# Kernel optimization log

Hardware: AMD Instinct MI355X
Metric: run time of the kernel (lower is better)

The kernel has to match this reference:

```python
import jax, jax.numpy as jnp
import numpy as np

B, Q, A, D = 32, 48, 48, 300   # batch, question len, answer len, word embed dim
C, K = 512, 5                  # conv out channels, kernel height
H, P, NCLS = 512, 512, 2       # hidden_size, projection_size, n_classes
EPS_COS = 1e-6
EPS_BN = 1e-5


def _simple_cnn(x, conv_w, conv_b, fc_w, fc_b):
    # x: (N, L, D) -> Conv2d(1->C, kernel=(K, D), padding=(K-1, 0)) -> relu -> maxpool over length -> fc
    y = jax.lax.conv_general_dilated(
        x[:, None, :, :], conv_w, window_strides=(1, 1),
        padding=((K - 1, K - 1), (0, 0)),
        dimension_numbers=('NCHW', 'OIHW', 'NCHW'))  # (N, C, L+K-1, 1)
    y = jax.nn.relu(y + conv_b[None, :, None, None])[..., 0]  # (N, C, L')
    y = jnp.max(y, axis=2)                                    # (N, C)  max_pool1d over full length
    return y @ fc_w.T + fc_b                                  # (N, H)


def setup_inputs() -> dict:
    key = jax.random.key(0)
    ks = jax.random.split(key, 12)
    s = lambda n: 1.0 / np.sqrt(n)
    return {
        'a_features': jax.random.normal(ks[0], (B, Q, D), jnp.float32),
        'b_features': jax.random.normal(ks[1], (B, A, D), jnp.float32),
        'sm_conv_w': jax.random.normal(ks[2], (C, 1, K, D), jnp.float32) * s(K * D),
        'sm_conv_b': jnp.zeros((C,), jnp.float32),
        'sm_fc_w': jax.random.normal(ks[3], (H, C), jnp.float32) * s(C),
        'sm_fc_b': jnp.zeros((H,), jnp.float32),
        'ctx_conv_w': jax.random.normal(ks[4], (C, 1, K, D), jnp.float32) * s(K * D),
        'ctx_conv_b': jnp.zeros((C,), jnp.float32),
        'ctx_fc_w': jax.random.normal(ks[5], (H, C), jnp.float32) * s(C),
        'ctx_fc_b': jnp.zeros((H,), jnp.float32),
        'proj_w': jax.random.normal(ks[6], (P, 3 * H), jnp.float32) * s(3 * H),
        'proj_b': jnp.zeros((P,), jnp.float32),
        'bn_gamma': jnp.ones((P,), jnp.float32),
        'bn_beta': jnp.zeros((P,), jnp.float32),
        'out_w': jax.random.normal(ks[7], (NCLS, P), jnp.float32) * s(P),
        'out_b': jnp.zeros((NCLS,), jnp.float32),
    }


def reference(a_features, b_features, sm_conv_w, sm_conv_b, sm_fc_w, sm_fc_b,
              ctx_conv_w, ctx_conv_b, ctx_fc_w, ctx_fc_b,
              proj_w, proj_b, bn_gamma, bn_beta, out_w, out_b):
    q, a = a_features, b_features
    a_cnn = _simple_cnn(q, sm_conv_w, sm_conv_b, sm_fc_w, sm_fc_b)  # (B, H)
    b_cnn = _simple_cnn(a, sm_conv_w, sm_conv_b, sm_fc_w, sm_fc_b)  # (B, H)

    # attn_context_ave: cosine sim between every (question pos, answer pos) pair
    qn = jnp.linalg.norm(q, axis=-1)                # (B, Q)
    an = jnp.linalg.norm(a, axis=-1)                # (B, A)
    dots = jnp.einsum('bqd,bad->bqa', q, a)
    cos = dots / jnp.maximum(qn[:, :, None] * an[:, None, :], EPS_COS)  # (B, Q, A)
    attn_answer = (a[:, None, :, :] * cos[..., None]).reshape(B * Q, A, D)
    feat = _simple_cnn(attn_answer, ctx_conv_w, ctx_conv_b, ctx_fc_w, ctx_fc_b)
    attn_feat = jnp.mean(feat.reshape(B, Q, H), axis=1)  # sum/Q == mean, (B, H)

    comb = jnp.concatenate([a_cnn, b_cnn, attn_feat], axis=1)  # (B, 3H)
    comb = comb @ proj_w.T + proj_b                            # (B, P)
    # BatchNorm1d in training mode (batch statistics, biased variance)
    mu = jnp.mean(comb, axis=0)
    var = jnp.mean((comb - mu) ** 2, axis=0)
    comb = (comb - mu) / jnp.sqrt(var + EPS_BN) * bn_gamma + bn_beta
    logits = jnp.tanh(comb) @ out_w.T + out_b                  # (B, NCLS)
    return logits
```

## Files before the change

kernel.cpp:

```cpp
#include <hip/hip_runtime.h>
#include <math.h>
#include <stdint.h>

namespace {
constexpr int B = 32, Q = 48, A = 48, D = 300;
constexpr int C = 512, K = 5, H = 512, P = 512, NCLS = 2;
constexpr int CK = C * K;
constexpr int M = B * Q;
constexpr int KP = 320;
constexpr float EPS_COS = 1e-6f, EPS_BN = 1e-5f;
constexpr int NPAN = 96 + 96 + 160 + 160;
constexpr int NCOS = M / 4;
constexpr int NJ = 8;
constexpr int PSZ = 40 * 16 * 8;
}
using short8 = __attribute__((ext_vector_type(8))) short;
using f32x4  = __attribute__((ext_vector_type(4))) float;

__device__ inline short f2bf(float v) {
  uint32_t u = __builtin_bit_cast(uint32_t, v);
  return (short)((u + 0x7fffu + ((u >> 16) & 1u)) >> 16);
}
__device__ inline float bf2f(short s) {
  uint32_t u = ((uint32_t)(uint16_t)s) << 16;
  return __builtin_bit_cast(float, u);
}

__global__ void prep_k(const float* __restrict__ q, const float* __restrict__ a,
                       const float* __restrict__ smw, const float* __restrict__ ctxw,
                       short* __restrict__ qb, short* __restrict__ ab,
                       short* __restrict__ smb, short* __restrict__ ctxb,
                       float* __restrict__ cosm) {
  __shared__ float4 qrow4[300];
  const int vb = blockIdx.x, tid = threadIdx.x;
  if (vb < NPAN) {
    const float* src; short* dst; int pl;
    if (vb < 96)       { src = q;    dst = qb;   pl = vb; }
    else if (vb < 192) { src = a;    dst = ab;   pl = vb - 96; }
    else if (vb < 352) { src = smw;  dst = smb;  pl = vb - 192; }
    else               { src = ctxw; dst = ctxb; pl = vb - 352; }
    const int row0 = pl * 16;
    for (int it = tid; it < 640; it += 256) {
      const int k8 = it >> 4, r = it & 15;
      short tmp[8];
#pragma unroll
      for (int e = 0; e < 8; ++e) {
        const int k = k8 * 8 + e;
        tmp[e] = (k < D) ? f2bf(src[(size_t)(row0 + r) * D + k]) : (short)0;
      }
      *(int4*)&dst[(size_t)pl * PSZ + (size_t)k8 * 128 + r * 8] = *(const int4*)tmp;
    }
  } else {
    const int b5 = vb - NPAN;
    const int qq = b5 * 4;
    const int b = qq / Q;
    const float4* qp4 = (const float4*)(q + (size_t)qq * D);
    for (int i = tid; i < 300; i += 256) qrow4[i] = qp4[i];
    __syncthreads();
    const int sub = tid >> 6, lane = tid & 63;
    float qsq = 0.f;
    for (int i = lane; i < 75; i += 64) {
      float4 v = qrow4[sub * 75 + i];
      qsq += v.x * v.x + v.y * v.y + v.z * v.z + v.w * v.w;
    }
#pragma unroll
    for (int off2 = 32; off2; off2 >>= 1) qsq += __shfl_xor(qsq, off2);
    const float qn = sqrtf(qsq);
    if (lane < A) {
      const float4* ap4 = (const float4*)(a + ((size_t)b * A + lane) * D);
      float dot = 0.f, asq = 0.f;
      for (int i = 0; i < 75; ++i) {
        float4 av = ap4[i], qv = qrow4[sub * 75 + i];
        dot += qv.x * av.x + qv.y * av.y + qv.z * av.z + qv.w * av.w;
        asq += av.x * av.x + av.y * av.y + av.z * av.z + av.w * av.w;
      }
      cosm[(size_t)(qq + sub) * A + lane] = dot / fmaxf(qn * sqrtf(asq), EPS_COS);
    }
  }
}

__global__ void __launch_bounds__(256)
fused_k(const short* __restrict__ qb, const short* __restrict__ ab,
        const short* __restrict__ smb, const short* __restrict__ ctxb,
        const float* __restrict__ cosm, const float* __restrict__ smbias,
        const float* __restrict__ ctxbias,
        const float* __restrict__ projw, const float* __restrict__ smfcw,
        const float* __restrict__ ctxfcw,
        float* __restrict__ projT, float* __restrict__ smfcwT,
        float* __restrict__ ctxfcwT,
        float* __restrict__ pooled, float* __restrict__ pbar) {
  __shared__ __align__(16) char Lraw[80000];
  const int vb = blockIdx.x, tid = threadIdx.x;

  if (vb >= 768) {
    float (*tile)[33] = (float (*)[33])Lraw;
    const int vb2 = vb - 768;
    const int tx = tid & 31, ty = tid >> 5;
    if (vb2 < 768) {
      const int j0 = (vb2 % 48) * 32, p0 = (vb2 / 48) * 32;
      for (int i = ty; i < 32; i += 8)
        tile[i][tx] = projw[(size_t)(p0 + i) * (3 * H) + j0 + tx];
      __syncthreads();
      for (int i = ty; i < 32; i += 8)
        projT[(size_t)(j0 + i) * P + p0 + tx] = tile[tx][i];
    } else {
      const int b3 = vb2 - 768;
      const bool isC = b3 >= 256;
      const int b4 = isC ? b3 - 256 : b3;
      const float* W = isC ? ctxfcw : smfcw;
      float* WT = isC ? ctxfcwT : smfcwT;
      const int c0 = (b4 % 16) * 32, h0 = (b4 / 16) * 32;
      for (int i = ty; i < 32; i += 8)
        tile[i][tx] = W[(size_t)(h0 + i) * C + c0 + tx];
      __syncthreads();
      for (int i = ty; i < 32; i += 8)
        WT[(size_t)(c0 + i) * H + h0 + tx] = tile[tx][i];
    }
    return;
  }

  float (*Sl)[56][81] = (float (*)[56][81])Lraw;
  short (*coslb)[56]  = (short (*)[56])(Lraw + 72576);
  float* redf         = (float*)(Lraw + 77952);
  const bool isCtx = vb < 256;
  const int v2 = isCtx ? vb : vb - 256;
  const int nb = v2 >> 3, cgi = v2 & 7;
  const int lane = tid & 63, wv = tid >> 6;
  const int r16 = lane & 15, kq = lane >> 4;

  const short* Xp = isCtx ? ab : ((nb < B) ? qb : ab);
  const int xp0 = (isCtx ? nb : ((nb < B) ? nb : nb - B)) * 3;
  const short* Wp = isCtx ? ctxb : smb;
  const int wp0 = cgi * 20 + wv * 5;
  const short* Xw = Xp + (size_t)xp0 * PSZ + kq * 128 + r16 * 8;
  const short* Ww = Wp + (size_t)wp0 * PSZ + kq * 128 + r16 * 8;

  for (int i = lane; i < 640; i += 64) {
    const int rr = i / 80, cc2 = i % 80;
    Sl[wv][rr < 4 ? rr : rr + 48][cc2] = 0.f;
  }
  if (isCtx) {
    for (int i = tid; i < 48 * 56; i += 256) {
      const int qi = i / 56, p4 = i % 56;
      const float cv = (p4 >= 4 && p4 < 52)
                     ? cosm[((size_t)nb * Q + qi) * A + p4 - 4] : 0.f;
      coslb[qi][p4] = f2bf(cv);
    }
  }

  f32x4 acc[3][5];
#pragma unroll
  for (int mi = 0; mi < 3; ++mi)
#pragma unroll
    for (int ni = 0; ni < 5; ++ni) acc[mi][ni] = f32x4{0.f, 0.f, 0.f, 0.f};
  int4 cA[3], cB[5];
#pragma unroll
  for (int i = 0; i < 3; ++i) cA[i] = *(const int4*)(Xw + (size_t)i * PSZ);
#pragma unroll
  for (int i = 0; i < 5; ++i) cB[i] = *(const int4*)(Ww + (size_t)i * PSZ);
#pragma unroll 1
  for (int ks = 0; ks < KP / 32; ++ks) {
    int4 nA[3], nB[5];
    if (ks < KP / 32 - 1) {
#pragma unroll
      for (int i = 0; i < 3; ++i) nA[i] = *(const int4*)(Xw + (size_t)i * PSZ + (ks + 1) * 512);
#pragma unroll
      for (int i = 0; i < 5; ++i) nB[i] = *(const int4*)(Ww + (size_t)i * PSZ + (ks + 1) * 512);
    }
#pragma unroll
    for (int mi = 0; mi < 3; ++mi)
#pragma unroll
      for (int ni = 0; ni < 5; ++ni)
        acc[mi][ni] = __builtin_amdgcn_mfma_f32_16x16x32_bf16(
            __builtin_bit_cast(short8, cA[mi]),
            __builtin_bit_cast(short8, cB[ni]), acc[mi][ni], 0, 0, 0);
    if (ks < KP / 32 - 1) {
#pragma unroll
      for (int i = 0; i < 3; ++i) cA[i] = nA[i];
#pragma unroll
      for (int i = 0; i < 5; ++i) cB[i] = nB[i];
    }
  }
#pragma unroll
  for (int mi = 0; mi < 3; ++mi)
#pragma unroll
    for (int ni = 0; ni < 5; ++ni)
#pragma unroll
      for (int r = 0; r < 4; ++r)
        Sl[wv][mi * 16 + kq * 4 + r + 4][ni * 16 + r16] = acc[mi][ni][r];
  __syncthreads();

  if (!isCtx) {
    const int ch = tid & 63, part = tid >> 6;
    const int w2 = ch >> 4, cl = (ch & 15) * 5;
    float best = -1e30f;
#pragma unroll
    for (int j = 0; j < 13; ++j) {
      const int l = part * 13 + j;
      const float z = Sl[w2][l + 0][cl + 0] + Sl[w2][l + 1][cl + 1]
                    + Sl[w2][l + 2][cl + 2] + Sl[w2][l + 3][cl + 3]
                    + Sl[w2][l + 4][cl + 4];
      best = fmaxf(best, z);
    }
    redf[part * 64 + ch] = best;
    __syncthreads();
    if (tid < 64) {
      const float m = fmaxf(fmaxf(redf[tid], redf[64 + tid]),
                            fmaxf(redf[128 + tid], redf[192 + tid]));
      pooled[(size_t)nb * C + cgi * 64 + tid] =
          fmaxf(m + smbias[cgi * 64 + tid], 0.f);
    }
  } else {
    const int clane = tid & 31, grp = tid >> 5;
    float best[2][6];
#pragma unroll
    for (int cc = 0; cc < 2; ++cc)
#pragma unroll
      for (int j = 0; j < 6; ++j) best[cc][j] = -1e30f;
    for (int ch13 = 0; ch13 < 13; ++ch13) {
      float cw[6][8];
#pragma unroll
      for (int j = 0; j < 6; ++j) {
        const short* crow = &coslb[grp * 6 + j][4 * ch13];
        const int2 w0 = *(const int2*)crow;
        const int2 w1 = *(const int2*)(crow + 4);
        cw[j][0] = __builtin_bit_cast(float, w0.x << 16);
        cw[j][1] = __builtin_bit_cast(float, (int)(w0.x & 0xffff0000));
        cw[j][2] = __builtin_bit_cast(float, w0.y << 16);
        cw[j][3] = __builtin_bit_cast(float, (int)(w0.y & 0xffff0000));
        cw[j][4] = __builtin_bit_cast(float, w1.x << 16);
        cw[j][5] = __builtin_bit_cast(float, (int)(w1.x & 0xffff0000));
        cw[j][6] = __builtin_bit_cast(float, w1.y << 16);
        cw[j][7] = __builtin_bit_cast(float, (int)(w1.y & 0xffff0000));
      }
#pragma unroll
      for (int cc = 0; cc < 2; ++cc) {
        const int ch = cc * 32 + clane;
        const int w2 = ch >> 4, cl = (ch & 15) * 5;
        float sk[4][5];
#pragma unroll
        for (int p = 0; p < 4; ++p)
#pragma unroll
          for (int k = 0; k < K; ++k)
            sk[p][k] = Sl[w2][4 * ch13 + p + k][cl + k];
#pragma unroll
        for (int p = 0; p < 4; ++p)
#pragma unroll
          for (int j = 0; j < 6; ++j) {
            float zv = 0.f;
#pragma unroll
            for (int k = 0; k < K; ++k) zv += cw[j][p + k] * sk[p][k];
            best[cc][j] = fmaxf(best[cc][j], zv);
          }
      }
    }
#pragma unroll
    for (int cc = 0; cc < 2; ++cc) {
      const float bc = ctxbias[cgi * 64 + cc * 32 + clane];
      float s = 0.f;
#pragma unroll
      for (int j = 0; j < 6; ++j) s += fmaxf(best[cc][j] + bc, 0.f);
      redf[cc * 256 + grp * 32 + clane] = s;
    }
    __syncthreads();
    if (tid < 64) {
      const int cc = tid >> 5, cl2 = tid & 31;
      float tot = 0.f;
#pragma unroll
      for (int g = 0; g < 8; ++g) tot += redf[cc * 256 + g * 32 + cl2];
      pbar[(size_t)nb * C + cgi * 64 + cc * 32 + cl2] = tot * (1.0f / Q);
    }
  }
}

__global__ void fc_k(const float* __restrict__ pooled, const float* __restrict__ pbar,
                     const float* __restrict__ smfcwT, const float* __restrict__ smfcb,
                     const float* __restrict__ ctxfcwT, const float* __restrict__ ctxfcb,
                     float* __restrict__ acnn, float* __restrict__ bcnn,
                     float* __restrict__ attnf) {
  __shared__ float row[C];
  const int vb = blockIdx.x, tid = threadIdx.x;
  const int n = vb / 6, rem = vb % 6, z = rem >> 1, hc = rem & 1;
  const int h = hc * 256 + tid;
  const float* in = (z == 0) ? pooled + (size_t)n * C
                  : (z == 1) ? pooled + (size_t)(B + n) * C
                             : pbar + (size_t)n * C;
  const float* WT = (z == 2) ? ctxfcwT : smfcwT;
  const float* bs = (z == 2) ? ctxfcb : smfcb;
  float* outp = ((z == 0) ? acnn : (z == 1) ? bcnn : attnf) + (size_t)n * H;
  for (int c = tid; c < C; c += 256) row[c] = in[c];
  __syncthreads();
  float acc = bs[h];
  for (int c = 0; c < C; ++c) acc += row[c] * WT[(size_t)c * H + h];
  outp[h] = acc;
}

__global__ void proj_k(const float* __restrict__ acnn, const float* __restrict__ bcnn,
                       const float* __restrict__ attnf, const float* __restrict__ WT,
                       float* __restrict__ partial) {
  __shared__ float cs[192];
  const int b = blockIdx.x, g = blockIdx.y, tid = threadIdx.x;
  const int js = g * 192;
  if (tid < 192) {
    const int j = js + tid;
    float v;
    if (j < H)          v = acnn[(size_t)b * H + j];
    else if (j < 2 * H) v = bcnn[(size_t)b * H + j - H];
    else                v = attnf[(size_t)b * H + j - 2 * H];
    cs[tid] = v;
  }
  __syncthreads();
  float a0 = 0.f, a1 = 0.f;
  for (int j = 0; j < 192; ++j) {
    const float c = cs[j];
    a0 += c * WT[(size_t)(js + j) * P + tid];
    a1 += c * WT[(size_t)(js + j) * P + tid + 256];
  }
  partial[((size_t)g * B + b) * P + tid] = a0;
  partial[((size_t)g * B + b) * P + tid + 256] = a1;
}

__global__ void bnmid_k(const float* __restrict__ partial, const float* __restrict__ proj_b,
                        const float* __restrict__ gamma, const float* __restrict__ beta,
                        float* __restrict__ t) {
  __shared__ float s1[256], s2[256];
  const int pl = threadIdx.x & 63, rg = threadIdx.x >> 6;
  const int p = blockIdx.x * 64 + pl;
  const float pb = proj_b[p];
  float v[8];
#pragma unroll
  for (int i = 0; i < 8; ++i) {
    const int r = rg * 8 + i;
    float s = pb;
#pragma unroll
    for (int g = 0; g < NJ; ++g) s += partial[((size_t)g * B + r) * P + p];
    v[i] = s;
  }
  float a = 0.f;
#pragma unroll
  for (int i = 0; i < 8; ++i) a += v[i];
  s1[rg * 64 + pl] = a;
  __syncthreads();
  const float mu = (s1[pl] + s1[64 + pl] + s1[128 + pl] + s1[192 + pl]) * (1.0f / B);
  float b2 = 0.f;
#pragma unroll
  for (int i = 0; i < 8; ++i) { const float d = v[i] - mu; b2 += d * d; }
  s2[rg * 64 + pl] = b2;
  __syncthreads();
  const float var = (s2[pl] + s2[64 + pl] + s2[128 + pl] + s2[192 + pl]) * (1.0f / B);
  const float inv = rsqrtf(var + EPS_BN);
  const float g = gamma[p], be = beta[p];
#pragma unroll
  for (int i = 0; i < 8; ++i)
    t[(size_t)(rg * 8 + i) * P + p] = tanhf((v[i] - mu) * inv * g + be);
}

__global__ void out_k(const float* __restrict__ t, const float* __restrict__ W,
                      const float* __restrict__ bias, float* __restrict__ out) {
  const int tid = threadIdx.x;
  const int o = tid >> 3, lane8 = tid & 7;
  const int bb = o >> 1, cl = o & 1;
  float acc = 0.f;
  for (int j = lane8; j < P; j += 8) acc += t[(size_t)bb * P + j] * W[cl * P + j];
#pragma unroll
  for (int off = 4; off; off >>= 1) acc += __shfl_down(acc, off);
  if (lane8 == 0) out[bb * NCLS + cl] = acc + bias[cl];
}

extern "C" void kernel_launch(void* const* d_in, const int* in_sizes, int n_in,
                              void* d_out, int out_size, void* d_ws, size_t ws_size,
                              hipStream_t stream) {
  const float* q       = (const float*)d_in[0];
  const float* a       = (const float*)d_in[1];
  const float* sm_w    = (const float*)d_in[2];
  const float* sm_b    = (const float*)d_in[3];
  const float* sm_fcw  = (const float*)d_in[4];
  const float* sm_fcb  = (const float*)d_in[5];
  const float* ctx_w   = (const float*)d_in[6];
  const float* ctx_b   = (const float*)d_in[7];
  const float* ctx_fcw = (const float*)d_in[8];
  const float* ctx_fcb = (const float*)d_in[9];
  const float* proj_w  = (const float*)d_in[10];
  const float* proj_b  = (const float*)d_in[11];
  const float* gamma   = (const float*)d_in[12];
  const float* beta    = (const float*)d_in[13];
  const float* out_w   = (const float*)d_in[14];
  const float* out_b   = (const float*)d_in[15];

  float* ws = (float*)d_ws;
  size_t off = 0;
  auto alloc = [&](size_t n) { float* p = ws + off; off += n; return p; };
  float* projT   = alloc((size_t)3 * H * P);
  float* smfcwT  = alloc((size_t)C * H);
  float* ctxfcwT = alloc((size_t)C * H);
  float* cosm    = alloc((size_t)B * Q * A);
  float* pooled  = alloc((size_t)2 * B * C);
  float* pbar    = alloc((size_t)B * C);
  float* acnn    = alloc((size_t)B * H);
  float* bcnn    = alloc((size_t)B * H);
  float* attnf   = alloc((size_t)B * H);
  float* partial = alloc((size_t)NJ * B * P);
  float* tbuf    = alloc((size_t)B * P);
  short* qb      = (short*)alloc((size_t)M * KP / 2);
  short* ab      = (short*)alloc((size_t)M * KP / 2);
  short* smb2    = (short*)alloc((size_t)CK * KP / 2);
  short* ctxb2   = (short*)alloc((size_t)CK * KP / 2);

  prep_k<<<NPAN + NCOS, 256, 0, stream>>>(q, a, sm_w, ctx_w, qb, ab, smb2, ctxb2, cosm);
  fused_k<<<2048, 256, 0, stream>>>(qb, ab, smb2, ctxb2, cosm, sm_b, ctx_b,
                                    proj_w, sm_fcw, ctx_fcw, projT, smfcwT, ctxfcwT,
                                    pooled, pbar);
  fc_k<<<192, 256, 0, stream>>>(pooled, pbar, smfcwT, sm_fcb, ctxfcwT, ctx_fcb,
                                acnn, bcnn, attnf);
  proj_k<<<dim3(B, NJ), 256, 0, stream>>>(acnn, bcnn, attnf, projT, partial);
  bnmid_k<<<P / 64, 256, 0, stream>>>(partial, proj_b, gamma, beta, tbuf);
  out_k<<<1, 512, 0, stream>>>(tbuf, out_w, out_b, (float*)d_out);
}
```

Before: 89.89 us.

## Fuse fc into projection kernel, double-buffer MFMA loads, stage prep via LDS

Merges the fc and projection kernels into one launch: each block computes the 192 fc outputs it needs and then applies its slice of the projection, which removes one launch and the intermediate acnn/bcnn/attnf buffers. The GEMM inner loop becomes two register buffers with the loop fully unrolled, so each step's loads overlap the other buffer's MFMAs. The prep kernel now stages each 16-row panel through shared memory with float4 loads before converting to bf16. In exchange, the fc work is recomputed once per batch row and group, and the extra register and LDS use may lower occupancy.

```diff
diff --git a/kernel.cpp b/kernel.cpp
--- a/kernel.cpp
+++ b/kernel.cpp
@@ -21,16 +21,13 @@
   uint32_t u = __builtin_bit_cast(uint32_t, v);
   return (short)((u + 0x7fffu + ((u >> 16) & 1u)) >> 16);
 }
-__device__ inline float bf2f(short s) {
-  uint32_t u = ((uint32_t)(uint16_t)s) << 16;
-  return __builtin_bit_cast(float, u);
-}
 
 __global__ void prep_k(const float* __restrict__ q, const float* __restrict__ a,
                        const float* __restrict__ smw, const float* __restrict__ ctxw,
                        short* __restrict__ qb, short* __restrict__ ab,
                        short* __restrict__ smb, short* __restrict__ ctxb,
                        float* __restrict__ cosm) {
+  __shared__ float sa[16 * 300];
   __shared__ float4 qrow4[300];
   const int vb = blockIdx.x, tid = threadIdx.x;
   if (vb < NPAN) {
@@ -40,13 +37,19 @@
     else if (vb < 352) { src = smw;  dst = smb;  pl = vb - 192; }
     else               { src = ctxw; dst = ctxb; pl = vb - 352; }
     const int row0 = pl * 16;
+    for (int i = tid; i < 1200; i += 256) {
+      const int r = i / 75, c4 = i - r * 75;
+      const float4 v = *(const float4*)&src[(size_t)(row0 + r) * D + c4 * 4];
+      *(float4*)&sa[r * 300 + c4 * 4] = v;
+    }
+    __syncthreads();
     for (int it = tid; it < 640; it += 256) {
       const int k8 = it >> 4, r = it & 15;
       short tmp[8];
 #pragma unroll
       for (int e = 0; e < 8; ++e) {
         const int k = k8 * 8 + e;
-        tmp[e] = (k < D) ? f2bf(src[(size_t)(row0 + r) * D + k]) : (short)0;
+        tmp[e] = (k < D) ? f2bf(sa[r * 300 + k]) : (short)0;
       }
       *(int4*)&dst[(size_t)pl * PSZ + (size_t)k8 * 128 + r * 8] = *(const int4*)tmp;
     }
@@ -153,33 +156,33 @@
   for (int mi = 0; mi < 3; ++mi)
 #pragma unroll
     for (int ni = 0; ni < 5; ++ni) acc[mi][ni] = f32x4{0.f, 0.f, 0.f, 0.f};
-  int4 cA[3], cB[5];
-#pragma unroll
-  for (int i = 0; i < 3; ++i) cA[i] = *(const int4*)(Xw + (size_t)i * PSZ);
-#pragma unroll
-  for (int i = 0; i < 5; ++i) cB[i] = *(const int4*)(Ww + (size_t)i * PSZ);
-#pragma unroll 1
-  for (int ks = 0; ks < KP / 32; ++ks) {
-    int4 nA[3], nB[5];
-    if (ks < KP / 32 - 1) {
-#pragma unroll
-      for (int i = 0; i < 3; ++i) nA[i] = *(const int4*)(Xw + (size_t)i * PSZ + (ks + 1) * 512);
-#pragma unroll
-      for (int i = 0; i < 5; ++i) nB[i] = *(const int4*)(Ww + (size_t)i * PSZ + (ks + 1) * 512);
-    }
+
+  int4 cA0[3], cB0[5], cA1[3], cB1[5];
+  auto issue = [&](int ks, int4* pA, int4* pB) {
+#pragma unroll
+    for (int i = 0; i < 3; ++i) pA[i] = *(const int4*)(Xw + (size_t)i * PSZ + ks * 512);
+#pragma unroll
+    for (int i = 0; i < 5; ++i) pB[i] = *(const int4*)(Ww + (size_t)i * PSZ + ks * 512);
+  };
+  auto domfma = [&](const int4* pA, const int4* pB) {
 #pragma unroll
     for (int mi = 0; mi < 3; ++mi)
 #pragma unroll
       for (int ni = 0; ni < 5; ++ni)
         acc[mi][ni] = __builtin_amdgcn_mfma_f32_16x16x32_bf16(
-            __builtin_bit_cast(short8, cA[mi]),
-            __builtin_bit_cast(short8, cB[ni]), acc[mi][ni], 0, 0, 0);
-    if (ks < KP / 32 - 1) {
-#pragma unroll
-      for (int i = 0; i < 3; ++i) cA[i] = nA[i];
-#pragma unroll
-      for (int i = 0; i < 5; ++i) cB[i] = nB[i];
-    }
+            __builtin_bit_cast(short8, pA[mi]),
+            __builtin_bit_cast(short8, pB[ni]), acc[mi][ni], 0, 0, 0);
+  };
+
+  issue(0, cA0, cB0);
+  issue(1, cA1, cB1);
+#pragma unroll
+  for (int ks2 = 0; ks2 < 5; ++ks2) {
+    const int ks = 2 * ks2;
+    domfma(cA0, cB0);
+    if (ks + 2 < 10) issue(ks + 2, cA0, cB0);
+    domfma(cA1, cB1);
+    if (ks + 3 < 10) issue(ks + 3, cA1, cB1);
   }
 #pragma unroll
   for (int mi = 0; mi < 3; ++mi)
@@ -273,48 +276,35 @@
   }
 }
 
-__global__ void fc_k(const float* __restrict__ pooled, const float* __restrict__ pbar,
-                     const float* __restrict__ smfcwT, const float* __restrict__ smfcb,
-                     const float* __restrict__ ctxfcwT, const float* __restrict__ ctxfcb,
-                     float* __restrict__ acnn, float* __restrict__ bcnn,
-                     float* __restrict__ attnf) {
-  __shared__ float row[C];
-  const int vb = blockIdx.x, tid = threadIdx.x;
-  const int n = vb / 6, rem = vb % 6, z = rem >> 1, hc = rem & 1;
-  const int h = hc * 256 + tid;
-  const float* in = (z == 0) ? pooled + (size_t)n * C
-                  : (z == 1) ? pooled + (size_t)(B + n) * C
-                             : pbar + (size_t)n * C;
-  const float* WT = (z == 2) ? ctxfcwT : smfcwT;
-  const float* bs = (z == 2) ? ctxfcb : smfcb;
-  float* outp = ((z == 0) ? acnn : (z == 1) ? bcnn : attnf) + (size_t)n * H;
-  for (int c = tid; c < C; c += 256) row[c] = in[c];
-  __syncthreads();
-  float acc = bs[h];
-  for (int c = 0; c < C; ++c) acc += row[c] * WT[(size_t)c * H + h];
-  outp[h] = acc;
-}
-
-__global__ void proj_k(const float* __restrict__ acnn, const float* __restrict__ bcnn,
-                       const float* __restrict__ attnf, const float* __restrict__ WT,
-                       float* __restrict__ partial) {
+__global__ void projfc_k(const float* __restrict__ pooled, const float* __restrict__ pbar,
+                         const float* __restrict__ smfcwT, const float* __restrict__ smfcb,
+                         const float* __restrict__ ctxfcwT, const float* __restrict__ ctxfcb,
+                         const float* __restrict__ projT, float* __restrict__ partial) {
+  __shared__ float rows[3 * C];
   __shared__ float cs[192];
   const int b = blockIdx.x, g = blockIdx.y, tid = threadIdx.x;
+  for (int i = tid; i < C; i += 256) {
+    rows[i] = pooled[(size_t)b * C + i];
+    rows[C + i] = pooled[(size_t)(B + b) * C + i];
+    rows[2 * C + i] = pbar[(size_t)b * C + i];
+  }
+  __syncthreads();
+  if (tid < 192) {
+    const int j = g * 192 + tid;
+    const int seg = j >> 9, h = j & 511;
+    const float* WT = (seg == 2) ? ctxfcwT : smfcwT;
+    const float* in = rows + seg * C;
+    float acc = (seg == 2) ? ctxfcb[h] : smfcb[h];
+    for (int c = 0; c < C; ++c) acc += in[c] * WT[(size_t)c * H + h];
+    cs[tid] = acc;
+  }
+  __syncthreads();
   const int js = g * 192;
-  if (tid < 192) {
-    const int j = js + tid;
-    float v;
-    if (j < H)          v = acnn[(size_t)b * H + j];
-    else if (j < 2 * H) v = bcnn[(size_t)b * H + j - H];
-    else                v = attnf[(size_t)b * H + j - 2 * H];
-    cs[tid] = v;
-  }
-  __syncthreads();
   float a0 = 0.f, a1 = 0.f;
   for (int j = 0; j < 192; ++j) {
     const float c = cs[j];
-    a0 += c * WT[(size_t)(js + j) * P + tid];
-    a1 += c * WT[(size_t)(js + j) * P + tid + 256];
+    a0 += c * projT[(size_t)(js + j) * P + tid];
+    a1 += c * projT[(size_t)(js + j) * P + tid + 256];
   }
   partial[((size_t)g * B + b) * P + tid] = a0;
   partial[((size_t)g * B + b) * P + tid + 256] = a1;
@@ -396,9 +386,6 @@
   float* cosm    = alloc((size_t)B * Q * A);
   float* pooled  = alloc((size_t)2 * B * C);
   float* pbar    = alloc((size_t)B * C);
-  float* acnn    = alloc((size_t)B * H);
-  float* bcnn    = alloc((size_t)B * H);
-  float* attnf   = alloc((size_t)B * H);
   float* partial = alloc((size_t)NJ * B * P);
   float* tbuf    = alloc((size_t)B * P);
   short* qb      = (short*)alloc((size_t)M * KP / 2);
@@ -410,9 +397,8 @@
   fused_k<<<2048, 256, 0, stream>>>(qb, ab, smb2, ctxb2, cosm, sm_b, ctx_b,
                                     proj_w, sm_fcw, ctx_fcw, projT, smfcwT, ctxfcwT,
                                     pooled, pbar);
-  fc_k<<<192, 256, 0, stream>>>(pooled, pbar, smfcwT, sm_fcb, ctxfcwT, ctx_fcb,
-                                acnn, bcnn, attnf);
-  proj_k<<<dim3(B, NJ), 256, 0, stream>>>(acnn, bcnn, attnf, projT, partial);
+  projfc_k<<<dim3(B, NJ), 256, 0, stream>>>(pooled, pbar, smfcwT, sm_fcb,
+                                            ctxfcwT, ctx_fcb, projT, partial);
   bnmid_k<<<P / 64, 256, 0, stream>>>(partial, proj_b, gamma, beta, tbuf);
   out_k<<<1, 512, 0, stream>>>(tbuf, out_w, out_b, (float*)d_out);
 }
```

Result: faster. 83.30 us (-7.3%).
